# Optimization experiments

Measured on AMD Instinct MI355X. Metric: run time of the kernel, lower is better.

Reference implementation:

```python
import jax, jax.numpy as jnp
import numpy as np

HIDDEN = 2048
HEADS = 16
HEAD_DIM = HIDDEN // HEADS
INTER = 8192
EPS = 1e-6


def setup_inputs() -> dict:
    key = jax.random.key(0)
    ks = jax.random.split(key, 10)
    s = 0.02
    return {
        "hidden_states": jax.random.normal(ks[0], (2, 2048, HIDDEN), dtype=jnp.float32),
        "wq": jax.random.normal(ks[1], (HIDDEN, HIDDEN), dtype=jnp.float32) * s,
        "wk": jax.random.normal(ks[2], (HIDDEN, HIDDEN), dtype=jnp.float32) * s,
        "wv": jax.random.normal(ks[3], (HIDDEN, HIDDEN), dtype=jnp.float32) * s,
        "wo": jax.random.normal(ks[4], (HIDDEN, HIDDEN), dtype=jnp.float32) * s,
        "w_gate": jax.random.normal(ks[5], (HIDDEN, INTER), dtype=jnp.float32) * s,
        "w_up": jax.random.normal(ks[6], (HIDDEN, INTER), dtype=jnp.float32) * s,
        "w_down": jax.random.normal(ks[7], (INTER, HIDDEN), dtype=jnp.float32) * s,
        "ln1_w": jnp.ones((HIDDEN,), dtype=jnp.float32),
        "ln2_w": jnp.ones((HIDDEN,), dtype=jnp.float32),
    }


def rmsnorm(x, w):
    xf = x.astype(jnp.float32)
    var = jnp.mean(xf * xf, axis=-1, keepdims=True)
    return w * (xf * jax.lax.rsqrt(var + EPS)).astype(x.dtype)


def reference(hidden_states, wq, wk, wv, wo, w_gate, w_up, w_down, ln1_w, ln2_w):
    B, S, H = hidden_states.shape
    residual = hidden_states
    x = rmsnorm(hidden_states, ln1_w)
    # projections -> [B, heads, S, head_dim]
    def split_heads(t):
        return t.reshape(B, S, HEADS, HEAD_DIM).transpose(0, 2, 1, 3)
    q = split_heads(x @ wq)
    k = split_heads(x @ wk)
    v = split_heads(x @ wv)
    scores = jnp.einsum('bhqd,bhkd->bhqk', q, k) / jnp.sqrt(jnp.float32(HEAD_DIM))
    causal = jnp.triu(jnp.ones((S, S), dtype=bool), k=1)
    scores = jnp.where(causal, -jnp.inf, scores)
    attn = jax.nn.softmax(scores, axis=-1)
    out = jnp.einsum('bhqk,bhkd->bhqd', attn, v)
    out = out.transpose(0, 2, 1, 3).reshape(B, S, H) @ wo
    hidden_states = residual + out
    residual = hidden_states
    x = rmsnorm(hidden_states, ln2_w)
    mlp = (jax.nn.silu(x @ w_gate) * (x @ w_up)) @ w_down
    return residual + mlp
```

## Files before the change

kernel.cpp:

```cpp
#include <hip/hip_runtime.h>
#include <hip/hip_bf16.h>
#include <cstdint>
#include <cstddef>


typedef _Float16 f16;
typedef __attribute__((ext_vector_type(8))) _Float16 f16x8;
typedef __attribute__((ext_vector_type(4))) float f32x4;

#define HIDDEN   2048
#define NHEADS   16
#define HEAD_DIM 128
#define INTER    8192
#define BATCH    2
#define SEQ      2048
#define NTOK     (BATCH * SEQ)

__device__ __forceinline__ void async16(void* lds, const void* g) {
    __builtin_amdgcn_global_load_lds(
        (const __attribute__((address_space(1))) void*)g,
        (__attribute__((address_space(3))) void*)lds, 16, 0, 0);
}

__global__ __launch_bounds__(256)
void rmsnorm_f16(const float* __restrict__ x, const float* __restrict__ w,
                 f16* __restrict__ out)
{
    const int row = blockIdx.x;
    const int tid = threadIdx.x;
    const float* xr = x + (size_t)row * HIDDEN;
    float4 a = ((const float4*)xr)[tid * 2];
    float4 b = ((const float4*)xr)[tid * 2 + 1];
    float ss = a.x*a.x + a.y*a.y + a.z*a.z + a.w*a.w
             + b.x*b.x + b.y*b.y + b.z*b.z + b.w*b.w;
    #pragma unroll
    for (int m = 32; m; m >>= 1) ss += __shfl_xor(ss, m, 64);
    __shared__ float red[4];
    if ((tid & 63) == 0) red[tid >> 6] = ss;
    __syncthreads();
    float tot = red[0] + red[1] + red[2] + red[3];
    float rs = rsqrtf(tot * (1.0f / HIDDEN) + 1e-6f);
    float vals[8] = {a.x, a.y, a.z, a.w, b.x, b.y, b.z, b.w};
    const float* wp = w + tid * 8;
    f16x8 o;
    #pragma unroll
    for (int j = 0; j < 8; ++j) o[j] = (f16)(vals[j] * rs * wp[j]);
    *(f16x8*)(out + (size_t)row * HIDDEN + tid * 8) = o;
}

__global__ __launch_bounds__(256)
void transpose_to_f16(const float* __restrict__ W, f16* __restrict__ Wt,
                      int K, int N)
{
    __shared__ float t[32][33];
    const int tx = threadIdx.x, ty = threadIdx.y;
    const int n0 = blockIdx.x * 32, k0 = blockIdx.y * 32;
    #pragma unroll
    for (int i = 0; i < 4; ++i)
        t[ty + i * 8][tx] = W[(size_t)(k0 + ty + i * 8) * N + n0 + tx];
    __syncthreads();
    #pragma unroll
    for (int i = 0; i < 4; ++i)
        Wt[(size_t)(n0 + ty + i * 8) * K + k0 + tx] = (f16)t[tx][ty + i * 8];
}

template<int EPI>
__global__ __launch_bounds__(256)
void gemm_bt(const f16* __restrict__ A, const f16* __restrict__ Bt,
             int M, int N, int K,
             f16* __restrict__ outh, float* __restrict__ outf,
             const float* __restrict__ resid, const f16* __restrict__ mulin,
             float scale)
{
    __shared__ __align__(16) f16 sA[128 * 64];
    __shared__ __align__(16) f16 sB[128 * 64];
    const int tid  = threadIdx.x;
    const int lane = tid & 63;
    const int wave = tid >> 6;
    const int wr = wave >> 1, wc = wave & 1;
    const int tM = blockIdx.y * 128, tN = blockIdx.x * 128;
    const int r16 = lane & 15, kg = lane >> 4;

    f32x4 acc[4][4] = {};

    const int rowA = tM + (tid >> 3);
    const int rowB = tN + (tid >> 3);
    const int cOff = (tid & 7) * 8;
    char* sAb = (char*)sA;
    char* sBb = (char*)sB;

    for (int k0 = 0; k0 < K; k0 += 64) {
        __syncthreads();
        #pragma unroll
        for (int i = 0; i < 4; ++i) {
            async16(sAb + i * 4096 + tid * 16,
                    A  + (size_t)(rowA + i * 32) * K + k0 + cOff);
            async16(sBb + i * 4096 + tid * 16,
                    Bt + (size_t)(rowB + i * 32) * K + k0 + cOff);
        }
        __syncthreads();
        #pragma unroll
        for (int kk = 0; kk < 2; ++kk) {
            f16x8 af[4], bf[4];
            #pragma unroll
            for (int m = 0; m < 4; ++m)
                af[m] = *(const f16x8*)(sA + (wr * 64 + m * 16 + r16) * 64 + kk * 32 + kg * 8);
            #pragma unroll
            for (int n = 0; n < 4; ++n)
                bf[n] = *(const f16x8*)(sB + (wc * 64 + n * 16 + r16) * 64 + kk * 32 + kg * 8);
            #pragma unroll
            for (int m = 0; m < 4; ++m)
                #pragma unroll
                for (int n = 0; n < 4; ++n)
                    acc[m][n] = __builtin_amdgcn_mfma_f32_16x16x32_f16(
                        af[m], bf[n], acc[m][n], 0, 0, 0);
        }
    }

    #pragma unroll
    for (int m = 0; m < 4; ++m) {
        #pragma unroll
        for (int n = 0; n < 4; ++n) {
            #pragma unroll
            for (int r = 0; r < 4; ++r) {
                const int row = tM + wr * 64 + m * 16 + kg * 4 + r;
                const int col = tN + wc * 64 + n * 16 + r16;
                const float v = acc[m][n][r];
                if (EPI == 0) {
                    const int b = row >> 11, s2 = row & (SEQ - 1);
                    const int h = col >> 7,  d  = col & (HEAD_DIM - 1);
                    outh[(((size_t)(b * NHEADS + h)) * SEQ + s2) * HEAD_DIM + d] =
                        (f16)(v * scale);
                } else if (EPI == 1) {
                    const size_t idx = (size_t)row * N + col;
                    outf[idx] = resid[idx] + v;
                } else if (EPI == 2) {
                    const size_t idx = (size_t)row * N + col;
                    outh[idx] = (f16)(v / (1.0f + __expf(-v)));
                } else {
                    const size_t idx = (size_t)row * N + col;
                    outh[idx] = (f16)(v * (float)mulin[idx]);
                }
            }
        }
    }
}

__global__ __launch_bounds__(256)
void attn_causal(const f16* __restrict__ Q, const f16* __restrict__ Kp,
                 const f16* __restrict__ V, f16* __restrict__ out)
{
    __shared__ __align__(16) f16 sK [64 * 136];
    __shared__ __align__(16) f16 sVt[128 * 72];
    __shared__ __align__(16) f16 sP [4 * 16 * 72];

    const int tid  = threadIdx.x;
    const int lane = tid & 63, wave = tid >> 6;
    const int r16 = lane & 15, kg = lane >> 4;
    const int qt = blockIdx.x, bh = blockIdx.y;
    const size_t base = (size_t)bh * SEQ * HEAD_DIM;
    const int q0 = qt * 64 + wave * 16;

    f16x8 qf[4];
    #pragma unroll
    for (int kk = 0; kk < 4; ++kk)
        qf[kk] = *(const f16x8*)(Q + base + (size_t)(q0 + r16) * HEAD_DIM + kk * 32 + kg * 8);

    f32x4 o[8] = {};
    float mr[4] = {-1e30f, -1e30f, -1e30f, -1e30f};
    float lr[4] = {0.f, 0.f, 0.f, 0.f};
    int qrow[4];
    #pragma unroll
    for (int r = 0; r < 4; ++r) qrow[r] = q0 + kg * 4 + r;

    for (int kt = 0; kt <= qt; ++kt) {
        __syncthreads();
        #pragma unroll
        for (int i = 0; i < 4; ++i) {
            const int key = i * 16 + (tid >> 4);
            const int c8  = (tid & 15) * 8;
            *(f16x8*)(sK + key * 136 + c8) =
                *(const f16x8*)(Kp + base + (size_t)(kt * 64 + key) * HEAD_DIM + c8);
            f16x8 v8 = *(const f16x8*)(V + base + (size_t)(kt * 64 + key) * HEAD_DIM + c8);
            #pragma unroll
            for (int j = 0; j < 8; ++j) sVt[(c8 + j) * 72 + key] = v8[j];
        }
        __syncthreads();

        f32x4 s[4] = {};
        #pragma unroll
        for (int kk = 0; kk < 4; ++kk)
            #pragma unroll
            for (int n = 0; n < 4; ++n) {
                f16x8 kf = *(const f16x8*)(sK + (n * 16 + r16) * 136 + kk * 32 + kg * 8);
                s[n] = __builtin_amdgcn_mfma_f32_16x16x32_f16(qf[kk], kf, s[n], 0, 0, 0);
            }

        #pragma unroll
        for (int r = 0; r < 4; ++r) {
            float pv[4];
            float rowmax = -1e30f;
            #pragma unroll
            for (int n = 0; n < 4; ++n) {
                const int key = kt * 64 + n * 16 + r16;
                const float v = (key <= qrow[r]) ? s[n][r] : -1e30f;
                pv[n] = v;
                rowmax = fmaxf(rowmax, v);
            }
            #pragma unroll
            for (int msk = 8; msk; msk >>= 1)
                rowmax = fmaxf(rowmax, __shfl_xor(rowmax, msk, 64));
            const float nm = fmaxf(mr[r], rowmax);
            const float sc = __expf(mr[r] - nm);
            mr[r] = nm;
            float rsum = 0.f;
            #pragma unroll
            for (int n = 0; n < 4; ++n) {
                const float p = __expf(pv[n] - nm);
                rsum += p;
                sP[wave * 1152 + (kg * 4 + r) * 72 + n * 16 + r16] = (f16)p;
            }
            #pragma unroll
            for (int msk = 8; msk; msk >>= 1) rsum += __shfl_xor(rsum, msk, 64);
            lr[r] = lr[r] * sc + rsum;
            #pragma unroll
            for (int d = 0; d < 8; ++d) o[d][r] *= sc;
        }
        __syncthreads();

        #pragma unroll
        for (int kk = 0; kk < 2; ++kk) {
            f16x8 pf = *(const f16x8*)(sP + wave * 1152 + r16 * 72 + kk * 32 + kg * 8);
            #pragma unroll
            for (int d = 0; d < 8; ++d) {
                f16x8 vf = *(const f16x8*)(sVt + (d * 16 + r16) * 72 + kk * 32 + kg * 8);
                o[d] = __builtin_amdgcn_mfma_f32_16x16x32_f16(pf, vf, o[d], 0, 0, 0);
            }
        }
    }

    const int b = bh >> 4, h = bh & 15;
    #pragma unroll
    for (int r = 0; r < 4; ++r) {
        const float inv = 1.0f / lr[r];
        const int q = qt * 64 + wave * 16 + kg * 4 + r;
        const size_t rowb = ((size_t)(b * SEQ + q)) * HIDDEN + h * HEAD_DIM;
        #pragma unroll
        for (int d = 0; d < 8; ++d)
            out[rowb + d * 16 + r16] = (f16)(o[d][r] * inv);
    }
}

extern "C" void kernel_launch(void* const* d_in, const int* in_sizes, int n_in,
                              void* d_out, int out_size, void* d_ws, size_t ws_size,
                              hipStream_t stream)
{
    const float* hs  = (const float*)d_in[0];
    const float* wq  = (const float*)d_in[1];
    const float* wk  = (const float*)d_in[2];
    const float* wv  = (const float*)d_in[3];
    const float* wo  = (const float*)d_in[4];
    const float* wg  = (const float*)d_in[5];
    const float* wu  = (const float*)d_in[6];
    const float* wd  = (const float*)d_in[7];
    const float* ln1 = (const float*)d_in[8];
    const float* ln2 = (const float*)d_in[9];
    float* out = (float*)d_out;
    char*  ws  = (char*)d_ws;

    f16*   wqT   = (f16*)(ws + 0);
    f16*   wkT   = (f16*)(ws + 8388608);
    f16*   wvT   = (f16*)(ws + 16777216);
    f16*   woT   = (f16*)(ws + 25165824);
    f16*   wgT   = (f16*)(ws + 33554432);
    f16*   wuT   = (f16*)(ws + 67108864);
    f16*   wdT   = (f16*)(ws + 100663296);
    f16*   x1    = (f16*)(ws + 134217728);
    f16*   qb    = (f16*)(ws + 150994944);
    f16*   kb    = (f16*)(ws + 167772160);
    f16*   vb    = (f16*)(ws + 184549376);
    f16*   attnb = (f16*)(ws + 201326592);
    f16*   sg    = (f16*)(ws + 150994944);
    float* hid2  = (float*)(ws + 218103808);
    f16*   hbuf  = (f16*)(ws + 0);

    const dim3 tb(32, 8);
    const float qscale = 0.08838834764831845f;

    rmsnorm_f16<<<NTOK, 256, 0, stream>>>(hs, ln1, x1);

    transpose_to_f16<<<dim3(64, 64),  tb, 0, stream>>>(wq, wqT, HIDDEN, HIDDEN);
    transpose_to_f16<<<dim3(64, 64),  tb, 0, stream>>>(wk, wkT, HIDDEN, HIDDEN);
    transpose_to_f16<<<dim3(64, 64),  tb, 0, stream>>>(wv, wvT, HIDDEN, HIDDEN);
    transpose_to_f16<<<dim3(64, 64),  tb, 0, stream>>>(wo, woT, HIDDEN, HIDDEN);
    transpose_to_f16<<<dim3(256, 64), tb, 0, stream>>>(wg, wgT, HIDDEN, INTER);
    transpose_to_f16<<<dim3(256, 64), tb, 0, stream>>>(wu, wuT, HIDDEN, INTER);
    transpose_to_f16<<<dim3(64, 256), tb, 0, stream>>>(wd, wdT, INTER, HIDDEN);

    const dim3 gP(HIDDEN / 128, NTOK / 128);
    gemm_bt<0><<<gP, 256, 0, stream>>>(x1, wqT, NTOK, HIDDEN, HIDDEN,
                                       qb, nullptr, nullptr, nullptr, qscale);
    gemm_bt<0><<<gP, 256, 0, stream>>>(x1, wkT, NTOK, HIDDEN, HIDDEN,
                                       kb, nullptr, nullptr, nullptr, 1.0f);
    gemm_bt<0><<<gP, 256, 0, stream>>>(x1, wvT, NTOK, HIDDEN, HIDDEN,
                                       vb, nullptr, nullptr, nullptr, 1.0f);

    attn_causal<<<dim3(SEQ / 64, BATCH * NHEADS), 256, 0, stream>>>(qb, kb, vb, attnb);

    gemm_bt<1><<<gP, 256, 0, stream>>>(attnb, woT, NTOK, HIDDEN, HIDDEN,
                                       nullptr, hid2, hs, nullptr, 0.f);

    rmsnorm_f16<<<NTOK, 256, 0, stream>>>(hid2, ln2, x1);

    const dim3 gI(INTER / 128, NTOK / 128);
    gemm_bt<2><<<gI, 256, 0, stream>>>(x1, wgT, NTOK, INTER, HIDDEN,
                                       sg, nullptr, nullptr, nullptr, 0.f);
    gemm_bt<3><<<gI, 256, 0, stream>>>(x1, wuT, NTOK, INTER, HIDDEN,
                                       hbuf, nullptr, nullptr, sg, 0.f);
    gemm_bt<1><<<gP, 256, 0, stream>>>(hbuf, wdT, NTOK, HIDDEN, INTER,
                                       nullptr, out, hid2, nullptr, 0.f);
}
```

Baseline: 1.590 ms.

## Write V transposed from its GEMM, reverse attention tile order, prioritize MFMA

The V projection GEMM gets a new epilogue that writes V directly in [b,h,d,s] layout. The attention kernel can then fill its transposed V tile with vectorized 16-byte loads instead of per-element scalar LDS stores. The attention grid now processes query tiles in reverse order so the longest causal tiles start first, and s_setprio raises wave priority around the MFMA loops. One __syncthreads is removed because each wave reads only its own sP region. The trade-off is that the transposed epilogue makes the V GEMM's global stores strided and poorly coalesced.

Result: faster. 1.391 ms (-12.6%).

```diff
diff --git a/kernel.cpp b/kernel.cpp
--- a/kernel.cpp
+++ b/kernel.cpp
@@ -137,9 +137,14 @@
                 } else if (EPI == 2) {
                     const size_t idx = (size_t)row * N + col;
                     outh[idx] = (f16)(v / (1.0f + __expf(-v)));
-                } else {
+                } else if (EPI == 3) {
                     const size_t idx = (size_t)row * N + col;
                     outh[idx] = (f16)(v * (float)mulin[idx]);
+                } else {
+                    const int b = row >> 11, s2 = row & (SEQ - 1);
+                    const int h = col >> 7,  d  = col & (HEAD_DIM - 1);
+                    outh[(((size_t)(b * NHEADS + h)) * HEAD_DIM + d) * SEQ + s2] =
+                        (f16)v;
                 }
             }
         }
@@ -148,7 +153,7 @@
 
 __global__ __launch_bounds__(256)
 void attn_causal(const f16* __restrict__ Q, const f16* __restrict__ Kp,
-                 const f16* __restrict__ V, f16* __restrict__ out)
+                 const f16* __restrict__ Vt, f16* __restrict__ out)
 {
     __shared__ __align__(16) f16 sK [64 * 136];
     __shared__ __align__(16) f16 sVt[128 * 72];
@@ -157,8 +162,10 @@
     const int tid  = threadIdx.x;
     const int lane = tid & 63, wave = tid >> 6;
     const int r16 = lane & 15, kg = lane >> 4;
-    const int qt = blockIdx.x, bh = blockIdx.y;
-    const size_t base = (size_t)bh * SEQ * HEAD_DIM;
+    const int qt = gridDim.x - 1 - blockIdx.x;
+    const int bh = blockIdx.y;
+    const size_t base  = (size_t)bh * SEQ * HEAD_DIM;
+    const size_t baseT = (size_t)bh * HEAD_DIM * SEQ;
     const int q0 = qt * 64 + wave * 16;
 
     f16x8 qf[4];
@@ -181,13 +188,18 @@
             const int c8  = (tid & 15) * 8;
             *(f16x8*)(sK + key * 136 + c8) =
                 *(const f16x8*)(Kp + base + (size_t)(kt * 64 + key) * HEAD_DIM + c8);
-            f16x8 v8 = *(const f16x8*)(V + base + (size_t)(kt * 64 + key) * HEAD_DIM + c8);
-            #pragma unroll
-            for (int j = 0; j < 8; ++j) sVt[(c8 + j) * 72 + key] = v8[j];
+        }
+        #pragma unroll
+        for (int it = 0; it < 4; ++it) {
+            const int idx = it * 256 + tid;
+            const int d = idx >> 3, key0 = (idx & 7) * 8;
+            *(f16x8*)(sVt + d * 72 + key0) =
+                *(const f16x8*)(Vt + baseT + (size_t)d * SEQ + kt * 64 + key0);
         }
         __syncthreads();
 
         f32x4 s[4] = {};
+        __builtin_amdgcn_s_setprio(1);
         #pragma unroll
         for (int kk = 0; kk < 4; ++kk)
             #pragma unroll
@@ -195,6 +207,7 @@
                 f16x8 kf = *(const f16x8*)(sK + (n * 16 + r16) * 136 + kk * 32 + kg * 8);
                 s[n] = __builtin_amdgcn_mfma_f32_16x16x32_f16(qf[kk], kf, s[n], 0, 0, 0);
             }
+        __builtin_amdgcn_s_setprio(0);
 
         #pragma unroll
         for (int r = 0; r < 4; ++r) {
@@ -226,8 +239,8 @@
             #pragma unroll
             for (int d = 0; d < 8; ++d) o[d][r] *= sc;
         }
-        __syncthreads();
-
+
+        __builtin_amdgcn_s_setprio(1);
         #pragma unroll
         for (int kk = 0; kk < 2; ++kk) {
             f16x8 pf = *(const f16x8*)(sP + wave * 1152 + r16 * 72 + kk * 32 + kg * 8);
@@ -237,6 +250,7 @@
                 o[d] = __builtin_amdgcn_mfma_f32_16x16x32_f16(pf, vf, o[d], 0, 0, 0);
             }
         }
+        __builtin_amdgcn_s_setprio(0);
     }
 
     const int b = bh >> 4, h = bh & 15;
@@ -278,7 +292,7 @@
     f16*   x1    = (f16*)(ws + 134217728);
     f16*   qb    = (f16*)(ws + 150994944);
     f16*   kb    = (f16*)(ws + 167772160);
-    f16*   vb    = (f16*)(ws + 184549376);
+    f16*   vtb   = (f16*)(ws + 184549376);
     f16*   attnb = (f16*)(ws + 201326592);
     f16*   sg    = (f16*)(ws + 150994944);
     float* hid2  = (float*)(ws + 218103808);
@@ -302,10 +316,10 @@
                                        qb, nullptr, nullptr, nullptr, qscale);
     gemm_bt<0><<<gP, 256, 0, stream>>>(x1, wkT, NTOK, HIDDEN, HIDDEN,
                                        kb, nullptr, nullptr, nullptr, 1.0f);
-    gemm_bt<0><<<gP, 256, 0, stream>>>(x1, wvT, NTOK, HIDDEN, HIDDEN,
-                                       vb, nullptr, nullptr, nullptr, 1.0f);
-
-    attn_causal<<<dim3(SEQ / 64, BATCH * NHEADS), 256, 0, stream>>>(qb, kb, vb, attnb);
+    gemm_bt<4><<<gP, 256, 0, stream>>>(x1, wvT, NTOK, HIDDEN, HIDDEN,
+                                       vtb, nullptr, nullptr, nullptr, 1.0f);
+
+    attn_causal<<<dim3(SEQ / 64, BATCH * NHEADS), 256, 0, stream>>>(qb, kb, vtb, attnb);
 
     gemm_bt<1><<<gP, 256, 0, stream>>>(attnb, woT, NTOK, HIDDEN, HIDDEN,
                                        nullptr, hid2, hs, nullptr, 0.f);
```
